# Kernel tuning notes

Measured on AMD Instinct MI355X. Metric: run time of the kernel, lower is better.

## Reference

```python
import jax, jax.numpy as jnp
import numpy as np

HIDDEN = 768
FFN = 3072
E = 8
TOP_K = 2


def setup_inputs() -> dict:
    key = jax.random.key(0)
    k_x, k_r, k_w1, k_w2 = jax.random.split(key, 4)
    x = jax.random.normal(k_x, (1, 1024, HIDDEN), dtype=jnp.float32)
    # nn.Linear(hidden, E, bias=False): weight applied as x @ W^T; store as [H, E]
    bound = 1.0 / np.sqrt(HIDDEN)
    router_w = jax.random.uniform(k_r, (HIDDEN, E), minval=-bound, maxval=bound, dtype=jnp.float32)
    w1 = jax.random.normal(k_w1, (E, HIDDEN, FFN), dtype=jnp.float32) * 0.02
    w2 = jax.random.normal(k_w2, (E, FFN, HIDDEN), dtype=jnp.float32) * 0.02
    return {"x": x, "router_w": router_w, "w1": w1, "w2": w2}


def reference(x, router_w, w1, w2):
    B, T, H = x.shape
    xf = x.reshape(-1, H)                                  # [N, H]
    logits = xf @ router_w                                 # [N, E] (eval mode: no noise)
    probs = jax.nn.softmax(logits, axis=-1)
    top_v, top_i = jax.lax.top_k(probs, TOP_K)             # [N, K]
    top_v = top_v / jnp.sum(top_v, axis=-1, keepdims=True)  # renormalize top-k probs
    # Combine top-k weights into a dense per-expert gate; zero gates make the
    # dense per-expert computation mathematically identical to sparse dispatch.
    gates = jnp.sum(jax.nn.one_hot(top_i, E, dtype=xf.dtype) * top_v[..., None], axis=1)  # [N, E]
    h = jax.nn.gelu(jnp.einsum('nh,ehf->enf', xf, w1), approximate=False)  # [E, N, F]
    y = jnp.einsum('enf,efh->enh', h, w2)                  # [E, N, H]
    out = jnp.einsum('ne,enh->nh', gates, y)               # [N, H]
    return out.reshape(B, T, H)
```

## Files before the change

kernel.cpp:

```cpp
#include <hip/hip_runtime.h>
#include <cmath>

#define NTOK 1024
#define HD   768
#define FF   3072
#define NE   8
#define NSLOT (NTOK * 2)
#define BK   64

typedef unsigned short u16;
typedef unsigned int   u32;
typedef __bf16 bf16x8 __attribute__((ext_vector_type(8)));
typedef float  f32x4  __attribute__((ext_vector_type(4)));

__device__ __forceinline__ u16 f2bf(float f) {
  union { float f; u32 u; } v; v.f = f;
  u32 r = v.u + 0x7FFFu + ((v.u >> 16) & 1u);
  return (u16)(r >> 16);
}

__device__ __forceinline__ void load16(const void* g, void* l) {
  __builtin_amdgcn_global_load_lds(
      (const __attribute__((address_space(1))) u32*)g,
      (__attribute__((address_space(3))) u32*)l, 16, 0, 0);
}

__global__ __launch_bounds__(256) void convert_t_kernel(
    const float* __restrict__ w1, const float* __restrict__ w2,
    u16* __restrict__ w1t, u16* __restrict__ w2t)
{
  const int z = blockIdx.z;
  const float* src; u16* dst; int K, N, n0, k0;
  if (z < NE) {
    src = w1 + (size_t)z * HD * FF; dst = w1t + (size_t)z * FF * HD;
    K = HD; N = FF; n0 = blockIdx.x * 64; k0 = blockIdx.y * 64;
  } else {
    src = w2 + (size_t)(z - NE) * FF * HD; dst = w2t + (size_t)(z - NE) * HD * FF;
    K = FF; N = HD; n0 = blockIdx.y * 64; k0 = blockIdx.x * 64;
  }
  __shared__ u16 lt[64][65];
  const int tid = threadIdx.x;
  const int rr = tid >> 4;
  const int cc = (tid & 15) << 2;
#pragma unroll
  for (int j = 0; j < 4; ++j) {
    const int k = j * 16 + rr;
    const float4 v = *(const float4*)(src + (size_t)(k0 + k) * N + n0 + cc);
    lt[cc + 0][k] = f2bf(v.x); lt[cc + 1][k] = f2bf(v.y);
    lt[cc + 2][k] = f2bf(v.z); lt[cc + 3][k] = f2bf(v.w);
  }
  __syncthreads();
#pragma unroll
  for (int j = 0; j < 4; ++j) {
    const int n = j * 16 + rr;
    ushort4 o;
    o.x = lt[n][cc]; o.y = lt[n][cc + 1]; o.z = lt[n][cc + 2]; o.w = lt[n][cc + 3];
    *(ushort4*)(dst + (size_t)(n0 + n) * K + k0 + cc) = o;
  }
}

__global__ __launch_bounds__(256) void router_logits(
    const float* __restrict__ x, const float* __restrict__ rw,
    u16* __restrict__ xb, int* __restrict__ counts,
    int* __restrict__ ti, int* __restrict__ tpos, float* __restrict__ tg)
{
  __shared__ float rwt[NE * HD];
  const int tid = threadIdx.x;
  for (int i = tid; i < NE * HD; i += 256) {
    const int h = i >> 3, e = i & 7;
    rwt[e * HD + h] = rw[i];
  }
  __syncthreads();

  const int wid  = tid >> 6;
  const int lane = tid & 63;
  const int t    = blockIdx.x * 4 + wid;
  const float* xrow = x + (size_t)t * HD;
  u16* xbrow = xb + (size_t)t * HD;

  float acc[NE] = {};
#pragma unroll
  for (int j = 0; j < 12; ++j) {
    const int h = lane + j * 64;
    const float xv = xrow[h];
    xbrow[h] = f2bf(xv);
#pragma unroll
    for (int e = 0; e < NE; ++e) acc[e] += xv * rwt[e * HD + h];
  }
#pragma unroll
  for (int e = 0; e < NE; ++e) {
    float v = acc[e];
#pragma unroll
    for (int off = 32; off; off >>= 1) v += __shfl_down(v, off, 64);
    acc[e] = v;
  }

  if (lane == 0) {
    float v0 = -1e30f, v1 = -1e30f; int i0 = 0, i1 = 0;
#pragma unroll
    for (int e = 0; e < NE; ++e) {
      const float p = acc[e];
      if (p > v0) { v1 = v0; i1 = i0; v0 = p; i0 = e; }
      else if (p > v1) { v1 = p; i1 = e; }
    }
    const float e1 = expf(v1 - v0);
    const float g0 = 1.0f / (1.0f + e1);
    const float g1 = e1 / (1.0f + e1);
    const int p0 = atomicAdd(&counts[i0], 1);
    const int p1 = atomicAdd(&counts[i1], 1);
    ti[2 * t] = i0;  ti[2 * t + 1] = i1;
    tpos[2 * t] = p0; tpos[2 * t + 1] = p1;
    tg[2 * t] = g0;  tg[2 * t + 1] = g1;
  }
}

__global__ __launch_bounds__(1024) void router_scatter(
    const int* __restrict__ counts, const int* __restrict__ ti,
    const int* __restrict__ tpos, const float* __restrict__ tg,
    int* __restrict__ tos, float* __restrict__ gos, int* __restrict__ seg)
{
  __shared__ int offs[NE];
  const int t = threadIdx.x;
  if (t == 0) {
    int o = 0;
    for (int e = 0; e < NE; ++e) {
      offs[e] = o; seg[e] = o; seg[NE + e] = counts[e]; o += counts[e];
    }
  }
  __syncthreads();
  const int i0 = ti[2 * t], i1 = ti[2 * t + 1];
  const int s0 = offs[i0] + tpos[2 * t];
  const int s1 = offs[i1] + tpos[2 * t + 1];
  tos[s0] = t; gos[s0] = tg[2 * t];
  tos[s1] = t; gos[s1] = tg[2 * t + 1];
}


__global__ __launch_bounds__(256) void ffn1_kernel(
    const u16* __restrict__ xb, const u16* __restrict__ w1t,
    const int* __restrict__ tos, const int* __restrict__ seg,
    u16* __restrict__ hbuf)
{
  const int e   = blockIdx.z;
  const int cnt = seg[NE + e];
  const int m0  = blockIdx.y * 128;
  if (m0 >= cnt) return;
  const int start = seg[e];
  const int n0    = blockIdx.x * 128;

  __shared__ __align__(16) u16 As[128 * 64];
  __shared__ __align__(16) u16 Bs[128 * 64];
  __shared__ int toks[128];

  const int tid = threadIdx.x;
  if (tid < 128) toks[tid] = tos[start + min(m0 + tid, cnt - 1)];
  __syncthreads();

  const int lane = tid & 63;
  const int wid  = tid >> 6;
  const int rsub = lane >> 3;
  const int c8   = (lane & 7) ^ rsub;

  const u16* ag[4]; const u16* bg[4];
  u16 *al[4], *bl[4];
#pragma unroll
  for (int i = 0; i < 4; ++i) {
    const int rb = wid * 8 + i * 32;
    ag[i] = xb + (size_t)toks[rb + rsub] * HD + c8 * 8;
    bg[i] = w1t + ((size_t)e * FF + n0 + rb + rsub) * HD + c8 * 8;
    al[i] = As + rb * 64;
    bl[i] = Bs + rb * 64;
  }

  const int wm  = (wid >> 1) << 6;
  const int wn  = (wid & 1) << 6;
  const int q   = lane >> 4;
  const int r16 = lane & 15;

  f32x4 acc[4][4] = {};

  for (int k0 = 0; k0 < HD; k0 += BK) {
#pragma unroll
    for (int i = 0; i < 4; ++i) {
      load16(ag[i] + k0, al[i]);
      load16(bg[i] + k0, bl[i]);
    }
    __syncthreads();
#pragma unroll
    for (int s = 0; s < 2; ++s) {
      const int pa = ((s << 2) + q) ^ (r16 & 7);
      bf16x8 af[4], bf[4];
#pragma unroll
      for (int t = 0; t < 4; ++t)
        af[t] = *(const bf16x8*)(&As[(wm + t * 16 + r16) * 64 + pa * 8]);
#pragma unroll
      for (int t = 0; t < 4; ++t)
        bf[t] = *(const bf16x8*)(&Bs[(wn + t * 16 + r16) * 64 + pa * 8]);
#pragma unroll
      for (int t = 0; t < 4; ++t)
#pragma unroll
        for (int c = 0; c < 4; ++c)
          acc[t][c] = __builtin_amdgcn_mfma_f32_16x16x32_bf16(af[t], bf[c], acc[t][c], 0, 0, 0);
    }
    __syncthreads();
  }

#pragma unroll
  for (int t = 0; t < 4; ++t) {
    const int mbase = m0 + wm + t * 16 + q * 4;
#pragma unroll
    for (int i = 0; i < 4; ++i) {
      if (mbase + i < cnt) {
        u16* drow = hbuf + (size_t)(start + mbase + i) * FF + n0 + wn;
#pragma unroll
        for (int c = 0; c < 4; ++c) {
          float v = acc[t][c][i];
          v = 0.5f * v * (1.0f + erff(v * 0.70710678118f));
          drow[c * 16 + r16] = f2bf(v);
        }
      }
    }
  }
}

#define KSPLIT 4
#define KSEG   (FF / KSPLIT)

__global__ __launch_bounds__(256) void ffn2_kernel(
    const u16* __restrict__ hbuf, const u16* __restrict__ w2t,
    const int* __restrict__ tos, const float* __restrict__ gos,
    const int* __restrict__ seg, float* __restrict__ out)
{
  const int ez  = blockIdx.z;
  const int e   = ez >> 2;
  const int ks  = ez & 3;
  const int cnt = seg[NE + e];
  const int m0  = blockIdx.y * 128;
  if (m0 >= cnt) return;
  const int start = seg[e];
  const int n0    = blockIdx.x * 128;
  const int kbase = ks * KSEG;

  __shared__ __align__(16) u16 As[128 * 64];
  __shared__ __align__(16) u16 Bs[128 * 64];
  __shared__ int   toks[128];
  __shared__ float gates[128];

  const int tid = threadIdx.x;
  if (tid < 128) {
    const int idx = start + min(m0 + tid, cnt - 1);
    toks[tid]  = tos[idx];
    gates[tid] = gos[idx];
  }
  __syncthreads();

  const int lane = tid & 63;
  const int wid  = tid >> 6;
  const int rsub = lane >> 3;
  const int c8   = (lane & 7) ^ rsub;

  const u16* ag[4]; const u16* bg[4];
  u16 *al[4], *bl[4];
#pragma unroll
  for (int i = 0; i < 4; ++i) {
    const int rb = wid * 8 + i * 32;
    ag[i] = hbuf + (size_t)(start + min(m0 + rb + rsub, cnt - 1)) * FF + kbase + c8 * 8;
    bg[i] = w2t + ((size_t)e * HD + n0 + rb + rsub) * FF + kbase + c8 * 8;
    al[i] = As + rb * 64;
    bl[i] = Bs + rb * 64;
  }

  const int wm  = (wid >> 1) << 6;
  const int wn  = (wid & 1) << 6;
  const int q   = lane >> 4;
  const int r16 = lane & 15;

  f32x4 acc[4][4] = {};

  for (int k0 = 0; k0 < KSEG; k0 += BK) {
#pragma unroll
    for (int i = 0; i < 4; ++i) {
      load16(ag[i] + k0, al[i]);
      load16(bg[i] + k0, bl[i]);
    }
    __syncthreads();
#pragma unroll
    for (int s = 0; s < 2; ++s) {
      const int pa = ((s << 2) + q) ^ (r16 & 7);
      bf16x8 af[4], bf[4];
#pragma unroll
      for (int t = 0; t < 4; ++t)
        af[t] = *(const bf16x8*)(&As[(wm + t * 16 + r16) * 64 + pa * 8]);
#pragma unroll
      for (int t = 0; t < 4; ++t)
        bf[t] = *(const bf16x8*)(&Bs[(wn + t * 16 + r16) * 64 + pa * 8]);
#pragma unroll
      for (int t = 0; t < 4; ++t)
#pragma unroll
        for (int c = 0; c < 4; ++c)
          acc[t][c] = __builtin_amdgcn_mfma_f32_16x16x32_bf16(af[t], bf[c], acc[t][c], 0, 0, 0);
    }
    __syncthreads();
  }

#pragma unroll
  for (int t = 0; t < 4; ++t) {
    const int mbase = wm + t * 16 + q * 4;
#pragma unroll
    for (int i = 0; i < 4; ++i) {
      const int mloc = mbase + i;
      if (m0 + mloc < cnt) {
        const int tok  = toks[mloc];
        const float g  = gates[mloc];
        float* drow = out + (size_t)tok * HD + n0 + wn;
#pragma unroll
        for (int c = 0; c < 4; ++c) {
          atomicAdd(drow + c * 16 + r16, g * acc[t][c][i]);
        }
      }
    }
  }
}

extern "C" void kernel_launch(void* const* d_in, const int* in_sizes, int n_in,
                              void* d_out, int out_size, void* d_ws, size_t ws_size,
                              hipStream_t stream) {
  const float* x  = (const float*)d_in[0];
  const float* rw = (const float*)d_in[1];
  const float* w1 = (const float*)d_in[2];
  const float* w2 = (const float*)d_in[3];
  float* out = (float*)d_out;

  char* ws = (char*)d_ws;
  const size_t o_xb    = 0;
  const size_t o_hbuf  = o_xb + (size_t)NTOK * HD * 2;
  const size_t o_tos   = o_hbuf + (size_t)NSLOT * FF * 2;
  const size_t o_gos   = o_tos + (size_t)NSLOT * 4;
  const size_t o_seg   = o_gos + (size_t)NSLOT * 4;
  const size_t o_cnt   = o_seg + 64 * 4;
  const size_t o_ti    = o_cnt + NE * 4;
  const size_t o_tpos  = o_ti + (size_t)NSLOT * 4;
  const size_t o_tg    = o_tpos + (size_t)NSLOT * 4;
  const size_t o_w1t   = (o_tg + (size_t)NSLOT * 4 + 255) & ~(size_t)255;
  const size_t o_w2t   = o_w1t + (size_t)NE * HD * FF * 2;
  u16*   xb    = (u16*)(ws + o_xb);
  u16*   hbuf  = (u16*)(ws + o_hbuf);
  int*   tos   = (int*)(ws + o_tos);
  float* gos   = (float*)(ws + o_gos);
  int*   seg   = (int*)(ws + o_seg);
  int*   cnts  = (int*)(ws + o_cnt);
  int*   ti    = (int*)(ws + o_ti);
  int*   tpos  = (int*)(ws + o_tpos);
  float* tg    = (float*)(ws + o_tg);
  u16*   w1t   = (u16*)(ws + o_w1t);
  u16*   w2t   = (u16*)(ws + o_w2t);

  hipMemsetAsync(d_out, 0, (size_t)NTOK * HD * sizeof(float), stream);
  hipMemsetAsync(cnts, 0, NE * sizeof(int), stream);
  hipLaunchKernelGGL(convert_t_kernel, dim3(48, 12, 2 * NE), dim3(256), 0, stream,
                     w1, w2, w1t, w2t);
  hipLaunchKernelGGL(router_logits, dim3(NTOK / 4), dim3(256), 0, stream,
                     x, rw, xb, cnts, ti, tpos, tg);
  hipLaunchKernelGGL(router_scatter, dim3(1), dim3(1024), 0, stream,
                     cnts, ti, tpos, tg, tos, gos, seg);
  hipLaunchKernelGGL(ffn1_kernel, dim3(FF / 128, NTOK / 128, NE), dim3(256), 0, stream,
                     xb, w1t, tos, seg, hbuf);
  hipLaunchKernelGGL(ffn2_kernel, dim3(HD / 128, NTOK / 128, NE * KSPLIT), dim3(256), 0, stream,
                     hbuf, w2t, tos, gos, seg, out);
}
```

Baseline: 300.6 us.

## Halve GEMM N-tile to 64 and widen transpose-convert tiles to 128 along K

Both FFN GEMM kernels now use 128x64 output tiles instead of 128x128, doubling the grid to fill more CUs, since most expert segments hold only a few hundred tokens. Each block also uses less LDS and fewer accumulator registers. The weight convert/transpose kernel now processes 64x128 tiles and writes 16-byte vector stores per thread rather than 8-byte ones, with a padded LDS stride. In exchange, the smaller GEMM tile reloads the A operand twice as often, and ffn2 issues more atomics per unit of work.

```diff
diff --git a/kernel.cpp b/kernel.cpp
--- a/kernel.cpp
+++ b/kernel.cpp
@@ -12,6 +12,7 @@
 typedef unsigned int   u32;
 typedef __bf16 bf16x8 __attribute__((ext_vector_type(8)));
 typedef float  f32x4  __attribute__((ext_vector_type(4)));
+typedef u16    u16x8  __attribute__((ext_vector_type(8)));
 
 __device__ __forceinline__ u16 f2bf(float f) {
   union { float f; u32 u; } v; v.f = f;
@@ -25,6 +26,8 @@
       (__attribute__((address_space(3))) u32*)l, 16, 0, 0);
 }
 
+#define CLD 130
+
 __global__ __launch_bounds__(256) void convert_t_kernel(
     const float* __restrict__ w1, const float* __restrict__ w2,
     u16* __restrict__ w1t, u16* __restrict__ w2t)
@@ -32,30 +35,41 @@
   const int z = blockIdx.z;
   const float* src; u16* dst; int K, N, n0, k0;
   if (z < NE) {
-    src = w1 + (size_t)z * HD * FF; dst = w1t + (size_t)z * FF * HD;
-    K = HD; N = FF; n0 = blockIdx.x * 64; k0 = blockIdx.y * 64;
+    src = w1 + (size_t)z * HD * FF;  dst = w1t + (size_t)z * FF * HD;
+    K = HD; N = FF;
+    n0 = blockIdx.x * 64;
+    k0 = blockIdx.y * 128;
   } else {
-    src = w2 + (size_t)(z - NE) * FF * HD; dst = w2t + (size_t)(z - NE) * HD * FF;
-    K = FF; N = HD; n0 = blockIdx.y * 64; k0 = blockIdx.x * 64;
-  }
-  __shared__ u16 lt[64][65];
+    src = w2 + (size_t)(z - NE) * FF * HD;  dst = w2t + (size_t)(z - NE) * HD * FF;
+    K = FF; N = HD;
+    k0 = (blockIdx.x % 24) * 128;
+    n0 = (blockIdx.y * 2 + blockIdx.x / 24) * 64;
+  }
+  __shared__ u16 lt[64 * CLD];
   const int tid = threadIdx.x;
   const int rr = tid >> 4;
   const int cc = (tid & 15) << 2;
 #pragma unroll
-  for (int j = 0; j < 4; ++j) {
+  for (int j = 0; j < 8; ++j) {
     const int k = j * 16 + rr;
     const float4 v = *(const float4*)(src + (size_t)(k0 + k) * N + n0 + cc);
-    lt[cc + 0][k] = f2bf(v.x); lt[cc + 1][k] = f2bf(v.y);
-    lt[cc + 2][k] = f2bf(v.z); lt[cc + 3][k] = f2bf(v.w);
-  }
-  __syncthreads();
-#pragma unroll
-  for (int j = 0; j < 4; ++j) {
-    const int n = j * 16 + rr;
-    ushort4 o;
-    o.x = lt[n][cc]; o.y = lt[n][cc + 1]; o.z = lt[n][cc + 2]; o.w = lt[n][cc + 3];
-    *(ushort4*)(dst + (size_t)(n0 + n) * K + k0 + cc) = o;
+    lt[(cc + 0) * CLD + k] = f2bf(v.x); lt[(cc + 1) * CLD + k] = f2bf(v.y);
+    lt[(cc + 2) * CLD + k] = f2bf(v.z); lt[(cc + 3) * CLD + k] = f2bf(v.w);
+  }
+  __syncthreads();
+  const int wn = tid >> 3;
+  const int kc = (tid & 7) << 4;
+#pragma unroll
+  for (int pass = 0; pass < 2; ++pass) {
+    const int n = wn + pass * 32;
+    u16x8 a, b;
+#pragma unroll
+    for (int d = 0; d < 8; ++d) a[d] = lt[n * CLD + kc + d];
+#pragma unroll
+    for (int d = 0; d < 8; ++d) b[d] = lt[n * CLD + kc + 8 + d];
+    u16* drow = dst + (size_t)(n0 + n) * K + k0 + kc;
+    *(u16x8*)(drow)     = a;
+    *(u16x8*)(drow + 8) = b;
   }
 }
 
@@ -146,10 +160,10 @@
   const int m0  = blockIdx.y * 128;
   if (m0 >= cnt) return;
   const int start = seg[e];
-  const int n0    = blockIdx.x * 128;
+  const int n0    = blockIdx.x * 64;
 
   __shared__ __align__(16) u16 As[128 * 64];
-  __shared__ __align__(16) u16 Bs[128 * 64];
+  __shared__ __align__(16) u16 Bs[64 * 64];
   __shared__ int toks[128];
 
   const int tid = threadIdx.x;
@@ -161,45 +175,48 @@
   const int rsub = lane >> 3;
   const int c8   = (lane & 7) ^ rsub;
 
-  const u16* ag[4]; const u16* bg[4];
-  u16 *al[4], *bl[4];
+  const u16* ag[4]; u16* al[4];
 #pragma unroll
   for (int i = 0; i < 4; ++i) {
     const int rb = wid * 8 + i * 32;
     ag[i] = xb + (size_t)toks[rb + rsub] * HD + c8 * 8;
+    al[i] = As + rb * 64;
+  }
+  const u16* bg[2]; u16* bl[2];
+#pragma unroll
+  for (int i = 0; i < 2; ++i) {
+    const int rb = wid * 8 + i * 32;
     bg[i] = w1t + ((size_t)e * FF + n0 + rb + rsub) * HD + c8 * 8;
-    al[i] = As + rb * 64;
     bl[i] = Bs + rb * 64;
   }
 
   const int wm  = (wid >> 1) << 6;
-  const int wn  = (wid & 1) << 6;
+  const int wn  = (wid & 1) << 5;
   const int q   = lane >> 4;
   const int r16 = lane & 15;
 
-  f32x4 acc[4][4] = {};
+  f32x4 acc[4][2] = {};
 
   for (int k0 = 0; k0 < HD; k0 += BK) {
 #pragma unroll
-    for (int i = 0; i < 4; ++i) {
-      load16(ag[i] + k0, al[i]);
-      load16(bg[i] + k0, bl[i]);
-    }
+    for (int i = 0; i < 4; ++i) load16(ag[i] + k0, al[i]);
+#pragma unroll
+    for (int i = 0; i < 2; ++i) load16(bg[i] + k0, bl[i]);
     __syncthreads();
 #pragma unroll
     for (int s = 0; s < 2; ++s) {
       const int pa = ((s << 2) + q) ^ (r16 & 7);
-      bf16x8 af[4], bf[4];
+      bf16x8 af[4], bf[2];
 #pragma unroll
       for (int t = 0; t < 4; ++t)
         af[t] = *(const bf16x8*)(&As[(wm + t * 16 + r16) * 64 + pa * 8]);
 #pragma unroll
+      for (int t = 0; t < 2; ++t)
+        bf[t] = *(const bf16x8*)(&Bs[(wn + t * 16 + r16) * 64 + pa * 8]);
+#pragma unroll
       for (int t = 0; t < 4; ++t)
-        bf[t] = *(const bf16x8*)(&Bs[(wn + t * 16 + r16) * 64 + pa * 8]);
-#pragma unroll
-      for (int t = 0; t < 4; ++t)
-#pragma unroll
-        for (int c = 0; c < 4; ++c)
+#pragma unroll
+        for (int c = 0; c < 2; ++c)
           acc[t][c] = __builtin_amdgcn_mfma_f32_16x16x32_bf16(af[t], bf[c], acc[t][c], 0, 0, 0);
     }
     __syncthreads();
@@ -213,7 +230,7 @@
       if (mbase + i < cnt) {
         u16* drow = hbuf + (size_t)(start + mbase + i) * FF + n0 + wn;
 #pragma unroll
-        for (int c = 0; c < 4; ++c) {
+        for (int c = 0; c < 2; ++c) {
           float v = acc[t][c][i];
           v = 0.5f * v * (1.0f + erff(v * 0.70710678118f));
           drow[c * 16 + r16] = f2bf(v);
@@ -238,11 +255,11 @@
   const int m0  = blockIdx.y * 128;
   if (m0 >= cnt) return;
   const int start = seg[e];
-  const int n0    = blockIdx.x * 128;
+  const int n0    = blockIdx.x * 64;
   const int kbase = ks * KSEG;
 
   __shared__ __align__(16) u16 As[128 * 64];
-  __shared__ __align__(16) u16 Bs[128 * 64];
+  __shared__ __align__(16) u16 Bs[64 * 64];
   __shared__ int   toks[128];
   __shared__ float gates[128];
 
@@ -259,45 +276,48 @@
   const int rsub = lane >> 3;
   const int c8   = (lane & 7) ^ rsub;
 
-  const u16* ag[4]; const u16* bg[4];
-  u16 *al[4], *bl[4];
+  const u16* ag[4]; u16* al[4];
 #pragma unroll
   for (int i = 0; i < 4; ++i) {
     const int rb = wid * 8 + i * 32;
     ag[i] = hbuf + (size_t)(start + min(m0 + rb + rsub, cnt - 1)) * FF + kbase + c8 * 8;
+    al[i] = As + rb * 64;
+  }
+  const u16* bg[2]; u16* bl[2];
+#pragma unroll
+  for (int i = 0; i < 2; ++i) {
+    const int rb = wid * 8 + i * 32;
     bg[i] = w2t + ((size_t)e * HD + n0 + rb + rsub) * FF + kbase + c8 * 8;
-    al[i] = As + rb * 64;
     bl[i] = Bs + rb * 64;
   }
 
   const int wm  = (wid >> 1) << 6;
-  const int wn  = (wid & 1) << 6;
+  const int wn  = (wid & 1) << 5;
   const int q   = lane >> 4;
   const int r16 = lane & 15;
 
-  f32x4 acc[4][4] = {};
+  f32x4 acc[4][2] = {};
 
   for (int k0 = 0; k0 < KSEG; k0 += BK) {
 #pragma unroll
-    for (int i = 0; i < 4; ++i) {
-      load16(ag[i] + k0, al[i]);
-      load16(bg[i] + k0, bl[i]);
-    }
+    for (int i = 0; i < 4; ++i) load16(ag[i] + k0, al[i]);
+#pragma unroll
+    for (int i = 0; i < 2; ++i) load16(bg[i] + k0, bl[i]);
     __syncthreads();
 #pragma unroll
     for (int s = 0; s < 2; ++s) {
       const int pa = ((s << 2) + q) ^ (r16 & 7);
-      bf16x8 af[4], bf[4];
+      bf16x8 af[4], bf[2];
 #pragma unroll
       for (int t = 0; t < 4; ++t)
         af[t] = *(const bf16x8*)(&As[(wm + t * 16 + r16) * 64 + pa * 8]);
 #pragma unroll
+      for (int t = 0; t < 2; ++t)
+        bf[t] = *(const bf16x8*)(&Bs[(wn + t * 16 + r16) * 64 + pa * 8]);
+#pragma unroll
       for (int t = 0; t < 4; ++t)
-        bf[t] = *(const bf16x8*)(&Bs[(wn + t * 16 + r16) * 64 + pa * 8]);
-#pragma unroll
-      for (int t = 0; t < 4; ++t)
-#pragma unroll
-        for (int c = 0; c < 4; ++c)
+#pragma unroll
+        for (int c = 0; c < 2; ++c)
           acc[t][c] = __builtin_amdgcn_mfma_f32_16x16x32_bf16(af[t], bf[c], acc[t][c], 0, 0, 0);
     }
     __syncthreads();
@@ -314,7 +334,7 @@
         const float g  = gates[mloc];
         float* drow = out + (size_t)tok * HD + n0 + wn;
 #pragma unroll
-        for (int c = 0; c < 4; ++c) {
+        for (int c = 0; c < 2; ++c) {
           atomicAdd(drow + c * 16 + r16, g * acc[t][c][i]);
         }
       }
@@ -357,14 +377,14 @@
 
   hipMemsetAsync(d_out, 0, (size_t)NTOK * HD * sizeof(float), stream);
   hipMemsetAsync(cnts, 0, NE * sizeof(int), stream);
-  hipLaunchKernelGGL(convert_t_kernel, dim3(48, 12, 2 * NE), dim3(256), 0, stream,
+  hipLaunchKernelGGL(convert_t_kernel, dim3(48, 6, 2 * NE), dim3(256), 0, stream,
                      w1, w2, w1t, w2t);
   hipLaunchKernelGGL(router_logits, dim3(NTOK / 4), dim3(256), 0, stream,
                      x, rw, xb, cnts, ti, tpos, tg);
   hipLaunchKernelGGL(router_scatter, dim3(1), dim3(1024), 0, stream,
                      cnts, ti, tpos, tg, tos, gos, seg);
-  hipLaunchKernelGGL(ffn1_kernel, dim3(FF / 128, NTOK / 128, NE), dim3(256), 0, stream,
+  hipLaunchKernelGGL(ffn1_kernel, dim3(FF / 64, NTOK / 128, NE), dim3(256), 0, stream,
                      xb, w1t, tos, seg, hbuf);
-  hipLaunchKernelGGL(ffn2_kernel, dim3(HD / 128, NTOK / 128, NE * KSPLIT), dim3(256), 0, stream,
+  hipLaunchKernelGGL(ffn2_kernel, dim3(HD / 64, NTOK / 128, NE * KSPLIT), dim3(256), 0, stream,
                      hbuf, w2t, tos, gos, seg, out);
 }
```

Result: faster. 281.4 us (-6.4%).
